# Optimization experiments

Hardware: AMD Instinct MI355X
Metric: run time of the kernel (lower is better)

The kernel has to match this reference:

```python
import jax, jax.numpy as jnp
import numpy as np

EPS = 1e-5
MIN_NORM = 1e-10

def _norm(x):
    return jnp.sqrt(jnp.clip(jnp.sum(x * x, axis=-1, keepdims=True), MIN_NORM, None))

def _proj(x):
    # clip points to the open unit Poincare ball
    n = _norm(x)
    max_n = 1.0 - EPS
    return jnp.where(n > max_n, x * (max_n / n), x)

def _artanh(x):
    return jnp.arctanh(jnp.clip(x, -1.0 + EPS, 1.0 - EPS))

def mob_add(u, v):
    uv = jnp.sum(u * v, axis=-1, keepdims=True)
    u2 = jnp.sum(u * u, axis=-1, keepdims=True)
    v2 = jnp.sum(v * v, axis=-1, keepdims=True)
    num = (1.0 + 2.0 * uv + v2) * u + (1.0 - u2) * v
    den = 1.0 + 2.0 * uv + u2 * v2
    return _proj(num / jnp.maximum(den, MIN_NORM))

def mob_mat_mul(M, x):
    # M: [Din, Dout], x: [B, Din] on the ball. Ganea Mobius matvec.
    x = _proj(x)
    Mx = x @ M
    x_n = _norm(x)
    Mx_n = _norm(Mx)
    return _proj(jnp.tanh(Mx_n / x_n * _artanh(x_n)) * (Mx / Mx_n))

def log_map_zero(y):
    n = _norm(y)
    return _artanh(n) * y / n

def exp_map_zero(v):
    n = _norm(v)
    return _proj(jnp.tanh(n) * v / n)

def mob_pointwise_prod(x, u):
    # coordinate-wise scale of hyperbolic x by gate u, in the tangent space at 0
    return exp_map_zero(log_map_zero(x) * u)

def _transition(W, h, U, x, b):
    Wh = mob_mat_mul(W, h)
    Ux = mob_mat_mul(U, x)
    return mob_add(mob_add(Wh, Ux), b)

def setup_inputs() -> dict:
    B, I, H = 2048, 1024, 1024
    Din, Dh = 2 * I, 2 * H
    k = (1.0 / H) ** 0.5
    key = jax.random.key(0)
    ks = jax.random.split(key, 8)
    return {
        "hyp_x": jax.random.normal(ks[0], (B, Din), jnp.float32) * 0.01,
        "hidden": jax.random.normal(ks[1], (B, Dh), jnp.float32) * 0.01,
        "w_z": jax.random.uniform(ks[2], (Dh, Dh), jnp.float32, -k, k),
        "w_r": jax.random.uniform(ks[3], (Dh, Dh), jnp.float32, -k, k),
        "w_h": jax.random.uniform(ks[4], (Dh, Dh), jnp.float32, -k, k),
        "u_z": jax.random.uniform(ks[5], (Din, Dh), jnp.float32, -k, k),
        "u_r": jax.random.uniform(ks[6], (Din, Dh), jnp.float32, -k, k),
        "b_z": jnp.zeros((Dh,), jnp.float32),
        "b_r": jnp.zeros((Dh,), jnp.float32),
        "b_h": jnp.zeros((Dh,), jnp.float32),
    }

def reference(hyp_x, hidden, w_z, w_r, w_h, u_z, u_r, b_z, b_r, b_h):
    hyp_x = _proj(hyp_x)
    hidden = _proj(hidden)
    z = jax.nn.sigmoid(log_map_zero(_transition(w_z, hidden, u_z, hyp_x, b_z)))
    r = jax.nn.sigmoid(log_map_zero(_transition(w_r, hidden, u_r, hyp_x, b_r)))
    r_point_h = mob_pointwise_prod(hidden, r)
    # NOTE: original source uses u_r (not u_h) here; replicated faithfully.
    h_tilde = _transition(w_h, r_point_h, u_r, hyp_x, b_h)
    minus_h_oplus_htilde = mob_add(-hidden, h_tilde)
    new_h = mob_add(hidden, mob_pointwise_prod(minus_h_oplus_htilde, z))
    return new_h
```

## Files before the change

### kernel.cpp

```cpp
#include <hip/hip_runtime.h>
#include <hip/hip_bf16.h>
#include <math.h>

#define EPS 1e-5f
#define MAXN (1.0f - EPS)
#define MINN 1e-10f

constexpr int D = 2048;

typedef unsigned short u16;
typedef __bf16 bf16x8 __attribute__((ext_vector_type(8)));
typedef float floatx4 __attribute__((ext_vector_type(4)));


__device__ __forceinline__ u16 f2bf(float f) {
    union { float f; unsigned u; } v; v.f = f;
    unsigned r = v.u + 0x7FFFu + ((v.u >> 16) & 1u);
    return (u16)(r >> 16);
}

__device__ __forceinline__ float bf2f(u16 b) {
    union { unsigned u; float f; } v; v.u = ((unsigned)b) << 16; return v.f;
}

__device__ __forceinline__ void load_bf8(const u16* p, float* d) {
    uint4 r = *(const uint4*)p;
    unsigned w[4] = {r.x, r.y, r.z, r.w};
    #pragma unroll
    for (int i = 0; i < 4; ++i) {
        d[2 * i]     = bf2f((u16)(w[i] & 0xFFFFu));
        d[2 * i + 1] = bf2f((u16)(w[i] >> 16));
    }
}

__device__ __forceinline__ void store_bf8(u16* p, const float* s) {
    u16 pk[8];
    #pragma unroll
    for (int i = 0; i < 8; ++i) pk[i] = f2bf(s[i]);
    *(uint4*)p = *(const uint4*)pk;
}

__device__ __forceinline__ void load_f8(const float* p, float* d) {
    *(float4*)(d)     = *(const float4*)(p);
    *(float4*)(d + 4) = *(const float4*)(p + 4);
}

__device__ __forceinline__ void store_f8(float* p, const float* s) {
    *(float4*)(p)     = *(const float4*)(s);
    *(float4*)(p + 4) = *(const float4*)(s + 4);
}

__device__ __forceinline__ float artanh_(float x) {
    x = fminf(fmaxf(x, -1.0f + EPS), 1.0f - EPS);
    return 0.5f * logf((1.0f + x) / (1.0f - x));
}

__device__ __forceinline__ float sigmoid_(float x) {
    return 1.0f / (1.0f + expf(-x));
}

__device__ __forceinline__ void gl_lds16(const u16* g, u16* l) {
    __builtin_amdgcn_global_load_lds(
        (const __attribute__((address_space(1))) unsigned int*)g,
        (__attribute__((address_space(3))) unsigned int*)l, 16, 0, 0);
}

template<int N>
__device__ __forceinline__ void block_sums(float* v, float* sbuf) {
    #pragma unroll
    for (int n = 0; n < N; ++n)
        #pragma unroll
        for (int off = 32; off >= 1; off >>= 1) v[n] += __shfl_xor(v[n], off, 64);
    int w = threadIdx.x >> 6;
    __syncthreads();
    if ((threadIdx.x & 63) == 0) {
        #pragma unroll
        for (int n = 0; n < N; ++n) sbuf[w * N + n] = v[n];
    }
    __syncthreads();
    #pragma unroll
    for (int n = 0; n < N; ++n)
        v[n] = sbuf[n] + sbuf[N + n] + sbuf[2 * N + n] + sbuf[3 * N + n];
}

__device__ __forceinline__ void mmm_finish(float sum2, float g, float* coef, float* onorm) {
    float mxn = sqrtf(fmaxf(sum2, MINN));
    float tt  = tanhf(mxn * g);
    float on  = fminf(tt, MAXN);
    *coef = on / mxn;
    *onorm = on;
}

__device__ __forceinline__ float mob_apply(float* u, const float* v,
                                           float u2, float v2, float duv) {
    float cu  = 1.f + 2.f * duv + v2;
    float cv  = 1.f - u2;
    float den = fmaxf(1.f + 2.f * duv + u2 * v2, MINN);
    float s2  = cu * cu * u2 + 2.f * cu * cv * duv + cv * cv * v2;
    float n   = sqrtf(fmaxf(s2 / (den * den), MINN));
    float sc  = ((n > MAXN) ? MAXN / n : 1.f) / den;
    #pragma unroll
    for (int i = 0; i < 8; ++i) u[i] = sc * (cu * u[i] + cv * v[i]);
    return fminf(n, MAXN);
}

__device__ __forceinline__ void trans_tile(const float* W, u16* Wt,
                                           int n0, int k0, float* tile) {
    int t = threadIdx.x;
    int lr = t >> 4, lc = (t & 15) * 4;
    #pragma unroll
    for (int p = 0; p < 4; ++p) {
        int r = lr + p * 16;
        float4 v = *(const float4*)(W + (size_t)(k0 + r) * D + n0 + lc);
        tile[r * 65 + lc + 0] = v.x;
        tile[r * 65 + lc + 1] = v.y;
        tile[r * 65 + lc + 2] = v.z;
        tile[r * 65 + lc + 3] = v.w;
    }
    __syncthreads();
    int wn = t >> 3, ws = (t & 7) * 8;
    #pragma unroll
    for (int p = 0; p < 2; ++p) {
        int n = wn + p * 32;
        u16 pk[8];
        #pragma unroll
        for (int j = 0; j < 8; ++j) pk[j] = f2bf(tile[(ws + j) * 65 + n]);
        *(uint4*)(Wt + (size_t)(n0 + n) * D + k0 + ws) = *(uint4*)pk;
    }
}


struct PrepBatch {
    const float* W[4]; u16* Wt[4];
    const float* hx; const float* h;
    u16* hx_bf; u16* h_bf;
    float* g_x; float* g_h;
};

__global__ __launch_bounds__(256) void wtrans_prep(PrepBatch pb) {
    __shared__ float tile[64 * 65];
    int t = threadIdx.x;

    if (blockIdx.z < 4) {
        trans_tile(pb.W[blockIdx.z], pb.Wt[blockIdx.z],
                   blockIdx.x * 64, blockIdx.y * 64, tile);
    } else {
        int bid = blockIdx.y * (D / 64) + blockIdx.x;
        for (int rr = 0; rr < 2; ++rr) {
            int b = bid * 2 + rr;
            size_t off = (size_t)b * D + t * 8;
            float xv[8], hv[8];
            load_f8(pb.hx + off, xv);
            load_f8(pb.h + off, hv);
            float s[2] = {0.f, 0.f};
            #pragma unroll
            for (int i = 0; i < 8; ++i) { s[0] += xv[i] * xv[i]; s[1] += hv[i] * hv[i]; }
            block_sums<2>(s, tile);

            float nx = sqrtf(fmaxf(s[0], MINN));
            float scx = (nx > MAXN) ? MAXN / nx : 1.0f;
            float nh = sqrtf(fmaxf(s[1], MINN));
            float sch = (nh > MAXN) ? MAXN / nh : 1.0f;
            #pragma unroll
            for (int i = 0; i < 8; ++i) { xv[i] *= scx; hv[i] *= sch; }
            store_bf8(pb.hx_bf + off, xv);
            store_bf8(pb.h_bf + off, hv);
            if (t == 0) {
                float xn = fminf(nx, MAXN), hn = fminf(nh, MAXN);
                pb.g_x[b] = artanh_(xn) / xn;
                pb.g_h[b] = artanh_(hn) / hn;
            }
        }
    }
}


template<int KLEN, typename CT>
__device__ __forceinline__ void gemm_body(const u16* __restrict__ A,
                                          const u16* __restrict__ W,
                                          CT* __restrict__ C, int koff,
                                          u16* As, u16* Ws) {
    int t = threadIdx.x;
    int wave = t >> 6, lane = t & 63;
    int wr = wave >> 1, wc = wave & 1;
    int quad = lane >> 4, l16 = lane & 15;
    int brow = blockIdx.y * 128, bcol = blockIdx.x * 128;

    int srow = 32 * wave + (lane >> 3);
    int sseg = (lane & 7) ^ ((lane >> 3) & 7);
    const u16* pa = A + (size_t)(brow + srow) * D + koff + sseg * 8;
    const u16* pw = W + (size_t)(bcol + srow) * D + koff + sseg * 8;
    u16* lbA = &As[wave * 2048];
    u16* lbW = &Ws[wave * 2048];

    floatx4 acc[4][4];
    #pragma unroll
    for (int i = 0; i < 4; ++i)
        #pragma unroll
        for (int j = 0; j < 4; ++j)
            #pragma unroll
            for (int e = 0; e < 4; ++e) acc[i][j][e] = 0.f;

    int xsw = l16 & 7;

    for (int k0 = 0; k0 < KLEN; k0 += 64) {
        __syncthreads();
        #pragma unroll
        for (int i = 0; i < 4; ++i) {
            gl_lds16(pa + (size_t)(8 * i) * D + k0, lbA + i * 512);
            gl_lds16(pw + (size_t)(8 * i) * D + k0, lbW + i * 512);
        }
        __syncthreads();

        #pragma unroll
        for (int kk = 0; kk < 2; ++kk) {
            bf16x8 af[4], bfv[4];
            int ps = ((kk * 4 + quad) ^ xsw) * 8;
            #pragma unroll
            for (int i = 0; i < 4; ++i)
                af[i] = *(const bf16x8*)(&As[(wr * 64 + i * 16 + l16) * 64 + ps]);
            #pragma unroll
            for (int j = 0; j < 4; ++j)
                bfv[j] = *(const bf16x8*)(&Ws[(wc * 64 + j * 16 + l16) * 64 + ps]);
            #pragma unroll
            for (int i = 0; i < 4; ++i)
                #pragma unroll
                for (int j = 0; j < 4; ++j)
                    acc[i][j] = __builtin_amdgcn_mfma_f32_16x16x32_bf16(af[i], bfv[j], acc[i][j], 0, 0, 0);
        }
    }

    #pragma unroll
    for (int i = 0; i < 4; ++i) {
        #pragma unroll
        for (int j = 0; j < 4; ++j) {
            int row = brow + wr * 64 + i * 16 + quad * 4;
            int col = bcol + wc * 64 + j * 16 + l16;
            #pragma unroll
            for (int r = 0; r < 4; ++r) {
                float val = acc[i][j][r];
                if constexpr (sizeof(CT) == 2)
                    C[(size_t)(row + r) * D + col] = (CT)f2bf(val);
                else
                    C[(size_t)(row + r) * D + col] = (CT)val;
            }
        }
    }
}


struct G1Batch {
    const u16* A[4]; const u16* W[4]; u16* C[4];
    const float* Wh; u16* WhT;
};

__global__ __launch_bounds__(256) void g1_kernel(G1Batch gb) {
    __shared__ u16 smem[128 * 64 * 2];
    if (blockIdx.z < 4) {
        gemm_body<2048, u16>(gb.A[blockIdx.z], gb.W[blockIdx.z], gb.C[blockIdx.z],
                             0, smem, smem + 128 * 64);
    } else {
        float* tile = (float*)smem;
        #pragma unroll
        for (int ti = 0; ti < 4; ++ti) {
            if (ti) __syncthreads();
            int n0 = (blockIdx.x * 2 + (ti & 1)) * 64;
            int k0 = (blockIdx.y * 2 + (ti >> 1)) * 64;
            trans_tile(gb.Wh, gb.WhT, n0, k0, tile);
        }
    }
}


struct GemmBatch { const u16* A[2]; const u16* W[2]; u16* C[2]; int koff[2]; };

__global__ __launch_bounds__(256) void g2_kernel(GemmBatch gb) {
    __shared__ u16 smem[128 * 64 * 2];
    int z = blockIdx.z;
    gemm_body<1024, u16>(gb.A[z], gb.W[z], gb.C[z], gb.koff[z],
                         smem, smem + 128 * 64);
}


__global__ __launch_bounds__(256) void mid_kernel(
    const u16* __restrict__ c_wz, const u16* __restrict__ c_uz,
    const u16* __restrict__ c_wr, const u16* __restrict__ c_ur,
    const u16* __restrict__ h_bf,
    const float* __restrict__ g_x, const float* __restrict__ g_h,
    const float* __restrict__ b_z, const float* __restrict__ b_r,
    u16* __restrict__ z_out, u16* __restrict__ uxr_out,
    u16* __restrict__ rph_bf, float* __restrict__ g_rph) {
    __shared__ float sbuf[24];
    int b = blockIdx.x, t = threadIdx.x;
    size_t off = (size_t)b * D + t * 8;
    int cbase = t * 8;

    float wz[8], uz[8], wr2[8], ur2[8], hp[8], bz[8], br[8];
    load_bf8(c_wz + off, wz);
    load_bf8(c_uz + off, uz);
    load_bf8(c_wr + off, wr2);
    load_bf8(c_ur + off, ur2);
    load_bf8(h_bf + off, hp);
    load_f8(b_z + cbase, bz);
    load_f8(b_r + cbase, br);

    float s[6] = {0, 0, 0, 0, 0, 0};
    #pragma unroll
    for (int i = 0; i < 8; ++i) {
        s[0] += wz[i] * wz[i];  s[1] += uz[i] * uz[i];
        s[2] += wr2[i] * wr2[i]; s[3] += ur2[i] * ur2[i];
        s[4] += bz[i] * bz[i];  s[5] += br[i] * br[i];
    }
    block_sums<6>(s, sbuf);
    float gh = g_h[b], gx = g_x[b];

    float cwz, nwz, cuz, nuz, cwr, nwr, cur, nur;
    mmm_finish(s[0], gh, &cwz, &nwz);
    mmm_finish(s[1], gx, &cuz, &nuz);
    mmm_finish(s[2], gh, &cwr, &nwr);
    mmm_finish(s[3], gx, &cur, &nur);
    #pragma unroll
    for (int i = 0; i < 8; ++i) {
        wz[i] *= cwz; uz[i] *= cuz; wr2[i] *= cwr; ur2[i] *= cur;
    }
    float sbz = s[4], sbr2 = s[5];

    float d[2] = {0.f, 0.f};
    #pragma unroll
    for (int i = 0; i < 8; ++i) { d[0] += wz[i] * uz[i]; d[1] += wr2[i] * ur2[i]; }
    block_sums<2>(d, sbuf);
    float n1z = mob_apply(wz, uz, nwz * nwz, nuz * nuz, d[0]);
    float n1r = mob_apply(wr2, ur2, nwr * nwr, nur * nur, d[1]);

    d[0] = 0.f; d[1] = 0.f;
    #pragma unroll
    for (int i = 0; i < 8; ++i) { d[0] += wz[i] * bz[i]; d[1] += wr2[i] * br[i]; }
    block_sums<2>(d, sbuf);
    float n2z = mob_apply(wz, bz, n1z * n1z, sbz, d[0]);
    float n2r = mob_apply(wr2, br, n1r * n1r, sbr2, d[1]);

    float gz = artanh_(n2z) / n2z;
    float gr = artanh_(n2r) / n2r;
    float zz[8], v[8];
    float sv = 0.f;
    #pragma unroll
    for (int i = 0; i < 8; ++i) {
        zz[i] = sigmoid_(gz * wz[i]);
        float r = sigmoid_(gr * wr2[i]);
        v[i] = gh * hp[i] * r;
        sv += v[i] * v[i];
    }
    store_bf8(z_out + off, zz);
    block_sums<1>(&sv, sbuf);
    float nv = sqrtf(fmaxf(sv, MINN));
    float th = fminf(tanhf(nv), MAXN);
    float cr = th / nv;
    #pragma unroll
    for (int i = 0; i < 8; ++i) v[i] *= cr;
    store_bf8(rph_bf + off, v);
    store_bf8(uxr_out + off, ur2);
    if (t == 0) g_rph[b] = artanh_(th) / th;
}


__global__ __launch_bounds__(256) void fin_kernel(
    const u16* __restrict__ p0, const u16* __restrict__ p1,
    const u16* __restrict__ uxr, const u16* __restrict__ z_in,
    const u16* __restrict__ h_bf,
    const float* __restrict__ g_rph, const float* __restrict__ b_h,
    float* __restrict__ out) {
    __shared__ float sbuf[16];
    int b = blockIdx.x, t = threadIdx.x;
    size_t off = (size_t)b * D + t * 8;
    int cbase = t * 8;

    float wh[8], ux[8], zz[8], hp[8], bh[8], t0[8];
    load_bf8(p0 + off, wh);
    load_bf8(p1 + off, t0);
    #pragma unroll
    for (int i = 0; i < 8; ++i) wh[i] += t0[i];
    load_bf8(uxr + off, ux);
    load_bf8(z_in + off, zz);
    load_bf8(h_bf + off, hp);
    load_f8(b_h + cbase, bh);

    float s[4] = {0, 0, 0, 0};
    #pragma unroll
    for (int i = 0; i < 8; ++i) {
        s[0] += wh[i] * wh[i]; s[1] += ux[i] * ux[i];
        s[2] += hp[i] * hp[i]; s[3] += bh[i] * bh[i];
    }
    block_sums<4>(s, sbuf);
    float swh = s[0], sux = s[1], shp = s[2], sbh = s[3];

    float cwh, nwh;
    mmm_finish(swh, g_rph[b], &cwh, &nwh);
    #pragma unroll
    for (int i = 0; i < 8; ++i) wh[i] *= cwh;

    float d = 0.f;
    #pragma unroll
    for (int i = 0; i < 8; ++i) d += wh[i] * ux[i];
    block_sums<1>(&d, sbuf);
    float n1 = mob_apply(wh, ux, nwh * nwh, sux, d);

    d = 0.f;
    #pragma unroll
    for (int i = 0; i < 8; ++i) d += wh[i] * bh[i];
    block_sums<1>(&d, sbuf);
    float nht = mob_apply(wh, bh, n1 * n1, sbh, d);

    #pragma unroll
    for (int i = 0; i < 8; ++i) ux[i] = -hp[i];
    d = 0.f;
    #pragma unroll
    for (int i = 0; i < 8; ++i) d += ux[i] * wh[i];
    block_sums<1>(&d, sbuf);
    float nm = mob_apply(ux, wh, shp, nht * nht, d);

    float lm = artanh_(nm) / nm;
    float sv = 0.f;
    #pragma unroll
    for (int i = 0; i < 8; ++i) {
        float v = lm * ux[i] * zz[i];
        ux[i] = v;
        sv += v * v;
    }
    block_sums<1>(&sv, sbuf);
    float nv = sqrtf(fmaxf(sv, MINN));
    float th = fminf(tanhf(nv), MAXN);
    float ce = th / nv;
    #pragma unroll
    for (int i = 0; i < 8; ++i) ux[i] *= ce;

    d = 0.f;
    #pragma unroll
    for (int i = 0; i < 8; ++i) d += hp[i] * ux[i];
    block_sums<1>(&d, sbuf);
    mob_apply(hp, ux, shp, th * th, d);
    store_f8(out + off, hp);
}


extern "C" void kernel_launch(void* const* d_in, const int* in_sizes, int n_in,
                              void* d_out, int out_size, void* d_ws, size_t ws_size,
                              hipStream_t stream) {
    const float* hyp_x  = (const float*)d_in[0];
    const float* hidden = (const float*)d_in[1];
    const float* w_z = (const float*)d_in[2];
    const float* w_r = (const float*)d_in[3];
    const float* w_h = (const float*)d_in[4];
    const float* u_z = (const float*)d_in[5];
    const float* u_r = (const float*)d_in[6];
    const float* b_z = (const float*)d_in[7];
    const float* b_r = (const float*)d_in[8];
    const float* b_h = (const float*)d_in[9];
    float* out = (float*)d_out;

    int B = in_sizes[1] / D;

    char* ws = (char*)d_ws;
    size_t o = 0;
    auto alloc = [&](size_t bytes) -> void* {
        void* p = ws + o;
        o += (bytes + 255) & ~(size_t)255;
        return p;
    };
    u16* wt[5];
    for (int i = 0; i < 5; ++i) wt[i] = (u16*)alloc((size_t)D * D * 2);
    u16* hx_bf = (u16*)alloc((size_t)B * D * 2);
    u16* h_bf  = (u16*)alloc((size_t)B * D * 2);
    float* g_x   = (float*)alloc((size_t)B * 4);
    float* g_h   = (float*)alloc((size_t)B * 4);
    float* g_rph = (float*)alloc((size_t)B * 4);
    u16* cz0 = (u16*)alloc((size_t)B * D * 2);
    u16* cz1 = (u16*)alloc((size_t)B * D * 2);
    u16* cz2 = (u16*)alloc((size_t)B * D * 2);
    u16* cz3 = (u16*)alloc((size_t)B * D * 2);
    u16* p0 = (u16*)alloc((size_t)B * D * 2);
    u16* p1 = (u16*)alloc((size_t)B * D * 2);
    u16* z_buf = (u16*)alloc((size_t)B * D * 2);
    u16* uxr = (u16*)alloc((size_t)B * D * 2);
    u16* rph = (u16*)alloc((size_t)B * D * 2);

    PrepBatch pb;
    pb.W[0] = w_z; pb.Wt[0] = wt[0];
    pb.W[1] = w_r; pb.Wt[1] = wt[1];
    pb.W[2] = u_z; pb.Wt[2] = wt[3];
    pb.W[3] = u_r; pb.Wt[3] = wt[4];
    pb.hx = hyp_x; pb.h = hidden;
    pb.hx_bf = hx_bf; pb.h_bf = h_bf;
    pb.g_x = g_x; pb.g_h = g_h;
    wtrans_prep<<<dim3(D / 64, D / 64, 5), 256, 0, stream>>>(pb);

    G1Batch g1;
    g1.A[0] = h_bf;  g1.W[0] = wt[0]; g1.C[0] = cz0;
    g1.A[1] = hx_bf; g1.W[1] = wt[3]; g1.C[1] = cz1;
    g1.A[2] = h_bf;  g1.W[2] = wt[1]; g1.C[2] = cz2;
    g1.A[3] = hx_bf; g1.W[3] = wt[4]; g1.C[3] = cz3;
    g1.Wh = w_h; g1.WhT = wt[2];
    g1_kernel<<<dim3(D / 128, B / 128, 5), 256, 0, stream>>>(g1);

    mid_kernel<<<dim3(B), 256, 0, stream>>>(cz0, cz1, cz2, cz3, h_bf, g_x, g_h,
                                            b_z, b_r, z_buf, uxr, rph, g_rph);

    GemmBatch g2;
    g2.A[0] = rph; g2.W[0] = wt[2]; g2.C[0] = p0; g2.koff[0] = 0;
    g2.A[1] = rph; g2.W[1] = wt[2]; g2.C[1] = p1; g2.koff[1] = 1024;
    g2_kernel<<<dim3(D / 128, B / 128, 2), 256, 0, stream>>>(g2);

    fin_kernel<<<dim3(B), 256, 0, stream>>>(p0, p1, uxr, z_buf, h_bf,
                                            g_rph, b_h, out);
}
```

Before: 299.1 us.

## Rewrite GEMMs as 256-tile double-buffered MFMA pipeline with priority-phased waves

Replaces the 128x128 single-buffered GEMM body with a 256-row tile, 8-wave (512-thread) kernel. It double-buffers LDS and issues global-to-LDS loads for the next k-tiles while the current MFMAs run, using s_setprio and barriers to phase compute against loads. The w_h transpose moves out of g1 into the prep kernel, so g1 is a pure GEMM launch. The aim is to hide memory latency and raise data reuse per block. In exchange it uses more LDS and registers per block and needs more complex vmcnt bookkeeping.

```diff
diff --git a/kernel.cpp b/kernel.cpp
--- a/kernel.cpp
+++ b/kernel.cpp
@@ -131,7 +131,7 @@
 
 
 struct PrepBatch {
-    const float* W[4]; u16* Wt[4];
+    const float* W[5]; u16* Wt[5];
     const float* hx; const float* h;
     u16* hx_bf; u16* h_bf;
     float* g_x; float* g_h;
@@ -141,8 +141,9 @@
     __shared__ float tile[64 * 65];
     int t = threadIdx.x;
 
-    if (blockIdx.z < 4) {
-        trans_tile(pb.W[blockIdx.z], pb.Wt[blockIdx.z],
+    if (blockIdx.z != 4) {
+        int wi = (blockIdx.z == 5) ? 4 : blockIdx.z;
+        trans_tile(pb.W[wi], pb.Wt[wi],
                    blockIdx.x * 64, blockIdx.y * 64, tile);
     } else {
         int bid = blockIdx.y * (D / 64) + blockIdx.x;
@@ -175,110 +176,186 @@
 }
 
 
-template<int KLEN, typename CT>
-__device__ __forceinline__ void gemm_body(const u16* __restrict__ A,
-                                          const u16* __restrict__ W,
-                                          CT* __restrict__ C, int koff,
-                                          u16* As, u16* Ws) {
-    int t = threadIdx.x;
-    int wave = t >> 6, lane = t & 63;
-    int wr = wave >> 1, wc = wave & 1;
-    int quad = lane >> 4, l16 = lane & 15;
-    int brow = blockIdx.y * 128, bcol = blockIdx.x * 128;
-
-    int srow = 32 * wave + (lane >> 3);
-    int sseg = (lane & 7) ^ ((lane >> 3) & 7);
-    const u16* pa = A + (size_t)(brow + srow) * D + koff + sseg * 8;
-    const u16* pw = W + (size_t)(bcol + srow) * D + koff + sseg * 8;
-    u16* lbA = &As[wave * 2048];
-    u16* lbW = &Ws[wave * 2048];
-
-    floatx4 acc[4][4];
-    #pragma unroll
-    for (int i = 0; i < 4; ++i)
+#define PHASE_MID() do { \
+    __builtin_amdgcn_s_barrier(); \
+    asm volatile("s_waitcnt lgkmcnt(0)" ::: "memory"); \
+    __builtin_amdgcn_sched_barrier(0); \
+    __builtin_amdgcn_s_setprio(1); } while (0)
+
+#define PHASE_END() do { \
+    __builtin_amdgcn_s_setprio(0); \
+    __builtin_amdgcn_s_barrier(); } while (0)
+
+template<int KLEN, int NJ>
+__device__ __forceinline__ void gemm256_body(const u16* __restrict__ A,
+                                             const u16* __restrict__ W,
+                                             u16* __restrict__ C, int koff,
+                                             u16* As, u16* Ws) {
+    constexpr int T  = KLEN / 64;
+    constexpr int BN = NJ * 64;
+    constexpr int AU = 8192;
+    constexpr int BU = BN * 32;
+
+    int t0 = threadIdx.x;
+    int wave = t0 >> 6, lane = t0 & 63, l16 = lane & 15, quad = lane >> 4;
+    int wr = wave >> 2, wc = wave & 3;
+    int brow = blockIdx.y * 256, bcol = blockIdx.x * BN;
+
+    int srow = t0 >> 2;
+    int sseg = (t0 & 3) ^ (srow & 3);
+    const u16* srcA = A + (size_t)(brow + srow) * D + koff + sseg * 8;
+    const u16* srcB = W + (size_t)(bcol + srow) * D + koff + sseg * 8;
+    u16* ldsA = As + wave * 512;
+    u16* ldsB = Ws + wave * 512;
+
+    auto stageA = [&](int buf, int kh, int tile) {
+        const u16* s = srcA + tile * 64 + kh * 32;
+        u16* d = ldsA + (buf * 2 + kh) * AU;
+        gl_lds16(s, d);
+        gl_lds16(s + (size_t)128 * D, d + 4096);
+    };
+    auto stageB = [&](int buf, int kh, int tile) {
+        const u16* s = srcB + tile * 64 + kh * 32;
+        u16* d = ldsB + (buf * 2 + kh) * BU;
+        gl_lds16(s, d);
+        if constexpr (NJ == 4) gl_lds16(s + (size_t)128 * D, d + 4096);
+    };
+
+    const u16* aF = As + (wr * 128 + l16) * 32 + ((quad ^ (l16 & 3)) * 8);
+    const u16* bF = Ws + (wc * (NJ * 16) + l16) * 32 + ((quad ^ (l16 & 3)) * 8);
+
+    floatx4 acc[8][NJ];
+    #pragma unroll
+    for (int i = 0; i < 8; ++i)
         #pragma unroll
-        for (int j = 0; j < 4; ++j)
+        for (int j = 0; j < NJ; ++j)
             #pragma unroll
             for (int e = 0; e < 4; ++e) acc[i][j][e] = 0.f;
 
-    int xsw = l16 & 7;
-
-    for (int k0 = 0; k0 < KLEN; k0 += 64) {
-        __syncthreads();
-        #pragma unroll
-        for (int i = 0; i < 4; ++i) {
-            gl_lds16(pa + (size_t)(8 * i) * D + k0, lbA + i * 512);
-            gl_lds16(pw + (size_t)(8 * i) * D + k0, lbW + i * 512);
-        }
-        __syncthreads();
-
-        #pragma unroll
-        for (int kk = 0; kk < 2; ++kk) {
-            bf16x8 af[4], bfv[4];
-            int ps = ((kk * 4 + quad) ^ xsw) * 8;
-            #pragma unroll
-            for (int i = 0; i < 4; ++i)
-                af[i] = *(const bf16x8*)(&As[(wr * 64 + i * 16 + l16) * 64 + ps]);
-            #pragma unroll
-            for (int j = 0; j < 4; ++j)
-                bfv[j] = *(const bf16x8*)(&Ws[(wc * 64 + j * 16 + l16) * 64 + ps]);
+    stageA(0, 0, 0); stageB(0, 0, 0);
+    stageA(0, 1, 0); stageB(0, 1, 0);
+    stageA(1, 0, 1); stageB(1, 0, 1);
+    if constexpr (NJ == 4) asm volatile("s_waitcnt vmcnt(4)" ::: "memory");
+    else                   asm volatile("s_waitcnt vmcnt(3)" ::: "memory");
+    __builtin_amdgcn_s_barrier();
+
+    #pragma unroll 2
+    for (int tt = 0; tt < T; ++tt) {
+        int bsel = tt & 1, bno = bsel ^ 1;
+        const u16* aT = aF + bsel * (2 * AU);
+        const u16* bT = bF + bsel * (2 * BU);
+        bool st1 = (tt + 1) < T, st2 = (tt + 2) < T;
+
+        if constexpr (NJ == 4) {
+            bf16x8 bfr[4], afr[4];
+            #pragma unroll
+            for (int j = 0; j < 4; ++j) bfr[j] = *(const bf16x8*)(bT + j * 512);
+            #pragma unroll
+            for (int i = 0; i < 4; ++i) afr[i] = *(const bf16x8*)(aT + i * 512);
+            if (st1) stageA(bno, 1, tt + 1);
+            PHASE_MID();
             #pragma unroll
             for (int i = 0; i < 4; ++i)
                 #pragma unroll
                 for (int j = 0; j < 4; ++j)
-                    acc[i][j] = __builtin_amdgcn_mfma_f32_16x16x32_bf16(af[i], bfv[j], acc[i][j], 0, 0, 0);
+                    acc[i][j] = __builtin_amdgcn_mfma_f32_16x16x32_bf16(afr[i], bfr[j], acc[i][j], 0, 0, 0);
+            PHASE_END();
+            #pragma unroll
+            for (int i = 0; i < 4; ++i) afr[i] = *(const bf16x8*)(aT + (4 + i) * 512);
+            if (st1) stageB(bno, 1, tt + 1);
+            PHASE_MID();
+            #pragma unroll
+            for (int i = 0; i < 4; ++i)
+                #pragma unroll
+                for (int j = 0; j < 4; ++j)
+                    acc[4 + i][j] = __builtin_amdgcn_mfma_f32_16x16x32_bf16(afr[i], bfr[j], acc[4 + i][j], 0, 0, 0);
+            PHASE_END();
+            #pragma unroll
+            for (int j = 0; j < 4; ++j) bfr[j] = *(const bf16x8*)(bT + BU + j * 512);
+            #pragma unroll
+            for (int i = 0; i < 4; ++i) afr[i] = *(const bf16x8*)(aT + AU + i * 512);
+            if (st2) stageA(bsel, 0, tt + 2);
+            PHASE_MID();
+            #pragma unroll
+            for (int i = 0; i < 4; ++i)
+                #pragma unroll
+                for (int j = 0; j < 4; ++j)
+                    acc[i][j] = __builtin_amdgcn_mfma_f32_16x16x32_bf16(afr[i], bfr[j], acc[i][j], 0, 0, 0);
+            PHASE_END();
+            #pragma unroll
+            for (int i = 0; i < 4; ++i) afr[i] = *(const bf16x8*)(aT + AU + (4 + i) * 512);
+            if (st2) stageB(bsel, 0, tt + 2);
+            PHASE_MID();
+            #pragma unroll
+            for (int i = 0; i < 4; ++i)
+                #pragma unroll
+                for (int j = 0; j < 4; ++j)
+                    acc[4 + i][j] = __builtin_amdgcn_mfma_f32_16x16x32_bf16(afr[i], bfr[j], acc[4 + i][j], 0, 0, 0);
+            __builtin_amdgcn_s_setprio(0);
+            asm volatile("s_waitcnt vmcnt(4)" ::: "memory");
+            __builtin_amdgcn_s_barrier();
+        } else {
+            bf16x8 bfr[2], afr[8];
+            #pragma unroll
+            for (int j = 0; j < 2; ++j) bfr[j] = *(const bf16x8*)(bT + j * 512);
+            #pragma unroll
+            for (int i = 0; i < 8; ++i) afr[i] = *(const bf16x8*)(aT + i * 512);
+            if (st1) { stageA(bno, 1, tt + 1); stageB(bno, 1, tt + 1); }
+            PHASE_MID();
+            #pragma unroll
+            for (int i = 0; i < 8; ++i)
+                #pragma unroll
+                for (int j = 0; j < 2; ++j)
+                    acc[i][j] = __builtin_amdgcn_mfma_f32_16x16x32_bf16(afr[i], bfr[j], acc[i][j], 0, 0, 0);
+            PHASE_END();
+            #pragma unroll
+            for (int j = 0; j < 2; ++j) bfr[j] = *(const bf16x8*)(bT + BU + j * 512);
+            #pragma unroll
+            for (int i = 0; i < 8; ++i) afr[i] = *(const bf16x8*)(aT + AU + i * 512);
+            if (st2) { stageA(bsel, 0, tt + 2); stageB(bsel, 0, tt + 2); }
+            PHASE_MID();
+            #pragma unroll
+            for (int i = 0; i < 8; ++i)
+                #pragma unroll
+                for (int j = 0; j < 2; ++j)
+                    acc[i][j] = __builtin_amdgcn_mfma_f32_16x16x32_bf16(afr[i], bfr[j], acc[i][j], 0, 0, 0);
+            __builtin_amdgcn_s_setprio(0);
+            asm volatile("s_waitcnt vmcnt(3)" ::: "memory");
+            __builtin_amdgcn_s_barrier();
         }
     }
 
     #pragma unroll
-    for (int i = 0; i < 4; ++i) {
+    for (int i = 0; i < 8; ++i) {
         #pragma unroll
-        for (int j = 0; j < 4; ++j) {
-            int row = brow + wr * 64 + i * 16 + quad * 4;
-            int col = bcol + wc * 64 + j * 16 + l16;
-            #pragma unroll
-            for (int r = 0; r < 4; ++r) {
-                float val = acc[i][j][r];
-                if constexpr (sizeof(CT) == 2)
-                    C[(size_t)(row + r) * D + col] = (CT)f2bf(val);
-                else
-                    C[(size_t)(row + r) * D + col] = (CT)val;
-            }
+        for (int j = 0; j < NJ; ++j) {
+            int row = brow + wr * 128 + i * 16 + quad * 4;
+            int col = bcol + wc * (NJ * 16) + j * 16 + l16;
+            #pragma unroll
+            for (int r = 0; r < 4; ++r)
+                C[(size_t)(row + r) * D + col] = f2bf(acc[i][j][r]);
         }
     }
 }
 
 
-struct G1Batch {
-    const u16* A[4]; const u16* W[4]; u16* C[4];
-    const float* Wh; u16* WhT;
-};
-
-__global__ __launch_bounds__(256) void g1_kernel(G1Batch gb) {
-    __shared__ u16 smem[128 * 64 * 2];
-    if (blockIdx.z < 4) {
-        gemm_body<2048, u16>(gb.A[blockIdx.z], gb.W[blockIdx.z], gb.C[blockIdx.z],
-                             0, smem, smem + 128 * 64);
-    } else {
-        float* tile = (float*)smem;
-        #pragma unroll
-        for (int ti = 0; ti < 4; ++ti) {
-            if (ti) __syncthreads();
-            int n0 = (blockIdx.x * 2 + (ti & 1)) * 64;
-            int k0 = (blockIdx.y * 2 + (ti >> 1)) * 64;
-            trans_tile(gb.Wh, gb.WhT, n0, k0, tile);
-        }
-    }
+struct G1Batch { const u16* A[4]; const u16* W[4]; u16* C[4]; };
+
+__global__ __launch_bounds__(512, 2) void g1_kernel(G1Batch gb) {
+    __shared__ u16 As[32768];
+    __shared__ u16 Ws[32768];
+    int z = blockIdx.z;
+    gemm256_body<2048, 4>(gb.A[z], gb.W[z], gb.C[z], 0, As, Ws);
 }
 
 
 struct GemmBatch { const u16* A[2]; const u16* W[2]; u16* C[2]; int koff[2]; };
 
-__global__ __launch_bounds__(256) void g2_kernel(GemmBatch gb) {
-    __shared__ u16 smem[128 * 64 * 2];
+__global__ __launch_bounds__(512, 2) void g2_kernel(GemmBatch gb) {
+    __shared__ u16 As[32768];
+    __shared__ u16 Ws[16384];
     int z = blockIdx.z;
-    gemm_body<1024, u16>(gb.A[z], gb.W[z], gb.C[z], gb.koff[z],
-                         smem, smem + 128 * 64);
+    gemm256_body<1024, 2>(gb.A[z], gb.W[z], gb.C[z], gb.koff[z], As, Ws);
 }
 
 
@@ -488,18 +565,18 @@
     pb.W[1] = w_r; pb.Wt[1] = wt[1];
     pb.W[2] = u_z; pb.Wt[2] = wt[3];
     pb.W[3] = u_r; pb.Wt[3] = wt[4];
+    pb.W[4] = w_h; pb.Wt[4] = wt[2];
     pb.hx = hyp_x; pb.h = hidden;
     pb.hx_bf = hx_bf; pb.h_bf = h_bf;
     pb.g_x = g_x; pb.g_h = g_h;
-    wtrans_prep<<<dim3(D / 64, D / 64, 5), 256, 0, stream>>>(pb);
+    wtrans_prep<<<dim3(D / 64, D / 64, 6), 256, 0, stream>>>(pb);
 
     G1Batch g1;
     g1.A[0] = h_bf;  g1.W[0] = wt[0]; g1.C[0] = cz0;
     g1.A[1] = hx_bf; g1.W[1] = wt[3]; g1.C[1] = cz1;
     g1.A[2] = h_bf;  g1.W[2] = wt[1]; g1.C[2] = cz2;
     g1.A[3] = hx_bf; g1.W[3] = wt[4]; g1.C[3] = cz3;
-    g1.Wh = w_h; g1.WhT = wt[2];
-    g1_kernel<<<dim3(D / 128, B / 128, 5), 256, 0, stream>>>(g1);
+    g1_kernel<<<dim3(D / 256, B / 256, 4), 512, 0, stream>>>(g1);
 
     mid_kernel<<<dim3(B), 256, 0, stream>>>(cz0, cz1, cz2, cz3, h_bf, g_x, g_h,
                                             b_z, b_r, z_buf, uxr, rph, g_rph);
@@ -507,7 +584,7 @@
     GemmBatch g2;
     g2.A[0] = rph; g2.W[0] = wt[2]; g2.C[0] = p0; g2.koff[0] = 0;
     g2.A[1] = rph; g2.W[1] = wt[2]; g2.C[1] = p1; g2.koff[1] = 1024;
-    g2_kernel<<<dim3(D / 128, B / 128, 2), 256, 0, stream>>>(g2);
+    g2_kernel<<<dim3(D / 128, B / 256, 2), 512, 0, stream>>>(g2);
 
     fin_kernel<<<dim3(B), 256, 0, stream>>>(p0, p1, uxr, z_buf, h_bf,
                                             g_rph, b_h, out);
```

After: 302.0 us. No clear change (+1.0%).
